# Performance work log

Hardware: AMD Instinct MI355X
Metric: run time of the kernel (lower is better)

The kernel has to match this reference:

```python
import jax, jax.numpy as jnp
import numpy as np

B, C, H, W = 16, 256, 56, 56
HID = C * 2            # modifier_expansion = 2
GROUPS = 8             # min(8, HID//4)
K = 3                  # inner_steps
LR = 0.01              # exp(log(inner_lr))
RATIO = 0.25           # spatial_mask_ratio
GN_EPS = 1e-5


def setup_inputs() -> dict:
    key = jax.random.key(0)
    ks = jax.random.split(key, 12)
    x = jax.random.normal(ks[0], (B, C, H, W), jnp.float32)
    # modifier params (1x1 convs stored as 2D matrices) + GroupNorm affine
    conv1_w = jax.random.normal(ks[1], (HID, C), jnp.float32) / np.sqrt(C)
    gn_gamma = 1.0 + 0.1 * jax.random.normal(ks[2], (HID,), jnp.float32)
    gn_beta = 0.1 * jax.random.normal(ks[3], (HID,), jnp.float32)
    conv2_w = jax.random.normal(ks[4], (C, HID), jnp.float32) / np.sqrt(HID)
    # surprise reconstructor (bottleneck = C//4)
    recon_w1 = jax.random.normal(ks[5], (C // 4, C), jnp.float32) / np.sqrt(C)
    recon_w2 = jax.random.normal(ks[6], (C, C // 4), jnp.float32) / np.sqrt(C // 4)
    # gate MLP
    gate_w1 = jax.random.normal(ks[7], (C // 4, C), jnp.float32) / np.sqrt(C)
    gate_b1 = jnp.zeros((C // 4,), jnp.float32)
    gate_w2 = jax.random.normal(ks[8], (1, C // 4), jnp.float32) / np.sqrt(C // 4)
    gate_b2 = jnp.zeros((1,), jnp.float32)
    residual_scale = jnp.asarray(0.05, jnp.float32)
    # EMA buffers (eval mode: frozen)
    running_mean = 0.05 * jax.random.normal(ks[9], (C,), jnp.float32)
    running_var = 1.0 + 0.05 * jax.random.uniform(ks[10], (C,), jnp.float32)
    # spatial masks: exactly int(H*W*RATIO) zeroed positions per sample, one mask
    # per inner update step (only steps 0..K-2 affect the output)
    num_mask = int(H * W * RATIO)
    rng = np.random.default_rng(0)
    r = rng.random((K - 1, B, H * W))
    idx = np.argsort(r, axis=-1)[..., :num_mask]
    m = np.ones((K - 1, B, H * W), dtype=bool)
    np.put_along_axis(m, idx, False, axis=-1)
    masks = jnp.asarray(m.reshape(K - 1, B, 1, H, W))
    return dict(x=x, conv1_w=conv1_w, gn_gamma=gn_gamma, gn_beta=gn_beta,
                conv2_w=conv2_w, recon_w1=recon_w1, recon_w2=recon_w2,
                gate_w1=gate_w1, gate_b1=gate_b1, gate_w2=gate_w2,
                gate_b2=gate_b2, residual_scale=residual_scale,
                running_mean=running_mean, running_var=running_var, masks=masks)


def _group_norm(h, gamma, beta):
    b = h.shape[0]
    hg = h.reshape(b, GROUPS, HID // GROUPS, H, W)
    mu = hg.mean(axis=(2, 3, 4), keepdims=True)
    var = hg.var(axis=(2, 3, 4), keepdims=True)  # biased, matching torch GN
    hg = (hg - mu) * jax.lax.rsqrt(var + GN_EPS)
    return hg.reshape(b, HID, H, W) * gamma[None, :, None, None] + beta[None, :, None, None]


def _modifier(feat, w1, gamma, beta, w2):
    # Conv2d 1x1 (no bias) -> GroupNorm -> GELU -> [Dropout2d: identity in eval] -> Conv2d 1x1
    h = jnp.einsum('bchw,oc->bohw', feat, w1)
    h = jax.nn.gelu(_group_norm(h, gamma, beta), approximate=False)
    return jnp.einsum('bohw,co->bchw', h, w2)


def _surprise(y, mask, rw1, rw2, rm, rv):
    mf = mask.astype(y.dtype)                       # [B,1,H,W]
    my = y * mf
    h = jax.nn.gelu(jnp.einsum('bchw,oc->bohw', my, rw1), approximate=False)
    rec = jnp.einsum('bohw,co->bchw', h, rw2)
    inv = 1.0 - mf
    recon = (((rec - y) ** 2) * inv).sum() / (inv.sum() * C + 1e-8)
    n = y.shape[0] * y.shape[2] * y.shape[3]
    cm = y.mean(axis=(0, 2, 3))                     # [C]
    cv = ((y - cm[None, :, None, None]) ** 2).sum(axis=(0, 2, 3)) / (n - 1)  # unbiased
    consist = ((cm - rm) ** 2).mean() + ((cv / (rv + 1e-8) - 1.0) ** 2).mean()
    return recon + 0.1 * consist


def reference(x, conv1_w, gn_gamma, gn_beta, conv2_w, recon_w1, recon_w2,
              gate_w1, gate_b1, gate_w2, gate_b2, residual_scale,
              running_mean, running_var, masks):
    feat = jax.lax.stop_gradient(x)  # feat_inner = features.detach()
    params = (conv1_w, gn_gamma, gn_beta, conv2_w)

    def inner_loss(p, mask):
        m = _modifier(feat, *p)
        return _surprise(m + feat, mask, recon_w1, recon_w2, running_mean, running_var)

    # TTT inner loop: K-1 SGD updates on the modifier params; updates are
    # stop_gradient'ed so the outer Jacobian wrt initial params is identity,
    # matching torch's .data in-place update with create_graph=False.
    for step in range(K - 1):
        g = jax.grad(inner_loss)(params, masks[step])
        params = tuple(p - LR * jax.lax.stop_gradient(gi) for p, gi in zip(params, g))

    modification = _modifier(x, *params)  # final forward uses non-detached features

    pooled = x.mean(axis=(2, 3))                                    # [B,C]
    gh = jax.nn.gelu(pooled @ gate_w1.T + gate_b1, approximate=False)
    gate = jax.nn.sigmoid(gh @ gate_w2.T + gate_b2)[:, :, None, None]  # [B,1,1,1]

    return x + residual_scale * gate * modification
```

## Files before the change

kernel.cpp:

```cpp
#include <hip/hip_runtime.h>
#include <math.h>


#define BB    16
#define CC    256
#define HWW   3136
#define NTOT  (BB*HWW)
#define HIDD  512
#define NGRP  8
#define GMSZ  (64*HWW)
#define C4    64
#define LRATE 0.01f
#define SKW   32
#define CHUNK (NTOT/SKW)
#define NV8   (HWW/8)
#define FSTR  132

#define EP_STORE    0
#define EP_ADDFEAT  1
#define EP_T1H      2
#define EP_DYREC    3
#define EP_DT1      4
#define EP_DYFIN    5
#define EP_H1STAT   6
#define EP_YADDSTAT 7
#define EP_GNB1     8
#define EP_OUT      9

typedef unsigned short u16;
typedef __attribute__((ext_vector_type(8))) short bf16x8;
typedef __attribute__((ext_vector_type(4))) float f32x4;

__device__ __forceinline__ float bf2f(u16 u){
  return __uint_as_float(((unsigned)u)<<16);
}
__device__ __forceinline__ u16 f2bf(float f){
  unsigned u = __float_as_uint(f);
  u += 0x7FFFu + ((u>>16)&1u);
  return (u16)(u>>16);
}
__device__ __forceinline__ float gelu_f(float x){
  return 0.5f*x*(1.0f+erff(x*0.70710678118654752f));
}
__device__ __forceinline__ float rcp_f(float x){ return __builtin_amdgcn_rcpf(x); }
__device__ __forceinline__ float gelu_fast(float x){
  float x2 = x*x;
  float u = 0.7978845608f*x*fmaf(0.044715f, x2, 1.0f);
  float t = 1.0f - 2.0f*rcp_f(__expf(2.0f*u)+1.0f);
  return 0.5f*x*(1.0f+t);
}
__device__ __forceinline__ float gelu_g_fast(float x){
  float x2 = x*x;
  float u = 0.7978845608f*x*fmaf(0.044715f, x2, 1.0f);
  float t = 1.0f - 2.0f*rcp_f(__expf(2.0f*u)+1.0f);
  float du = 0.7978845608f*fmaf(0.134145f, x2, 1.0f);
  return fmaf(0.5f*x*(1.0f-t*t), du, 0.5f*(1.0f+t));
}
__device__ __forceinline__ float blk_sum(float v, float* sm){
  #pragma unroll
  for (int o=32;o>0;o>>=1) v += __shfl_down(v,o);
  if ((threadIdx.x & 63)==0) sm[threadIdx.x>>6] = v;
  __syncthreads();
  float r = sm[0]+sm[1]+sm[2]+sm[3];
  __syncthreads();
  return r;
}
__device__ __forceinline__ uint4 pack8(const ushort* e){
  uint4 v;
  v.x = (unsigned)e[0] | ((unsigned)e[1]<<16);
  v.y = (unsigned)e[2] | ((unsigned)e[3]<<16);
  v.z = (unsigned)e[4] | ((unsigned)e[5]<<16);
  v.w = (unsigned)e[6] | ((unsigned)e[7]<<16);
  return v;
}
__device__ __forceinline__ void up8(uint4 v, float* f){
  f[0]=bf2f((u16)(v.x&0xFFFFu)); f[1]=bf2f((u16)(v.x>>16));
  f[2]=bf2f((u16)(v.y&0xFFFFu)); f[3]=bf2f((u16)(v.y>>16));
  f[4]=bf2f((u16)(v.z&0xFFFFu)); f[5]=bf2f((u16)(v.z>>16));
  f[6]=bf2f((u16)(v.w&0xFFFFu)); f[7]=bf2f((u16)(v.w>>16));
}
__device__ __forceinline__ uint4 pk8(const float* f){
  uint4 v;
  v.x=(unsigned)f2bf(f[0])|((unsigned)f2bf(f[1])<<16);
  v.y=(unsigned)f2bf(f[2])|((unsigned)f2bf(f[3])<<16);
  v.z=(unsigned)f2bf(f[4])|((unsigned)f2bf(f[5])<<16);
  v.w=(unsigned)f2bf(f[6])|((unsigned)f2bf(f[7])<<16);
  return v;
}

__global__ void k_detect_dtype(const u16* __restrict__ xs, int* flag){
  if (threadIdx.x || blockIdx.x) return;
  int plaus = 0;
  for (int i=0;i<256;i+=2){
    float f = bf2f(xs[i]);
    float a = fabsf(f);
    if (isfinite(f) && a < 32.0f && a > 1e-5f) plaus++;
  }
  *flag = (plaus >= 64) ? 1 : 0;
}
__global__ void k_detect_mask(const unsigned char* __restrict__ m, int* flag){
  if (threadIdx.x || blockIdx.x) return;
  unsigned char mx=0; int nz0=0,nz1=0,nz2=0,nz3=0;
  for (int i=0;i<256;i++){
    unsigned char v=m[i]; if (v>mx) mx=v;
    if (v){ int r=i&3; if(r==0)nz0=1; else if(r==1)nz1=1; else if(r==2)nz2=1; else nz3=1; }
  }
  int f;
  if (mx<=1) f = (nz1|nz2|nz3) ? 0 : 1;
  else       f = (!nz0 && !nz1) ? 3 : 2;
  *flag=f;
}
__global__ void k_report(u16* out, float v){
  if (threadIdx.x==0 && blockIdx.x==0) out[0] = f2bf(v);
}

__global__ void k_cvt(const void* __restrict__ src, float* __restrict__ dst, int n,
                      const int* __restrict__ dtf){
  int i = blockIdx.x*256 + threadIdx.x;
  if (i>=n) return;
  if (*dtf) dst[i] = bf2f(((const u16*)src)[i]);
  else      dst[i] = ((const float*)src)[i];
}
__global__ void k_wcvt(const float* __restrict__ src, u16* __restrict__ d,
                       u16* __restrict__ dT, int R, int Cc){
  int i = blockIdx.x*256+threadIdx.x;
  if (i >= R*Cc) return;
  int r = i/Cc, c = i - r*Cc;
  u16 v = f2bf(src[i]);
  d[i] = v;
  if (dT) dT[(size_t)c*R + r] = v;
}

__global__ void k_expand(const unsigned char* __restrict__ mraw, const int* __restrict__ flag,
                         float* __restrict__ mf, float* __restrict__ zc){
  __shared__ float sm[4];
  int i = blockIdx.x*256 + threadIdx.x;
  int f = *flag;
  float v;
  if (f==1)      v = (((const int*)mraw)[i] != 0) ? 1.f : 0.f;
  else if (f==0) v = (mraw[i] != 0) ? 1.f : 0.f;
  else if (f==2) v = (((const u16*)mraw)[i] != 0) ? 1.f : 0.f;
  else           v = (((const float*)mraw)[i] != 0.f) ? 1.f : 0.f;
  mf[i] = v;
  float S = blk_sum(1.f - v, sm);
  if (threadIdx.x==0) atomicAdd(&zc[blockIdx.x/196], S);
}

template<int MASKX,int EPI,int XDYN,int E0DYN,int XGN>
__global__ __launch_bounds__(256) void k_gemm_mfma(
    const u16* __restrict__ A, const void* __restrict__ Xv, u16* __restrict__ Out,
    int K, const int* __restrict__ xdt, const float* __restrict__ mf,
    const void* __restrict__ e0, const float* __restrict__ e1,
    const float* __restrict__ e2, u16* __restrict__ o2, float* __restrict__ o3,
    const float* __restrict__ xmu, const float* __restrict__ xpg)
{
  __shared__ __align__(16) u16 Ws[64*42];
  __shared__ __align__(16) u16 Xs[128*42];
  const int t = threadIdx.x;
  const int w = t >> 6, lane = t & 63;
  const int col = lane & 15, quad = lane >> 4;
  const int M = (int)gridDim.y << 6;
  const int m0 = blockIdx.y << 6, n0 = blockIdx.x << 7;
  const int isbx = XDYN ? *xdt : 1;
  const u16*   Xb = (const u16*)Xv;
  const float* Xf = (const float*)Xv;
  const int wrow = t >> 2, wkq = (t & 3) * 8;
  const int xn   = 2*(t & 63);
  const int xq   = t >> 6;
  const int gn0  = n0 + xn;
  const int xb_  = gn0 / HWW;
  const int xs_  = gn0 - xb_*HWW;

  f32x4 acc[4][2];
  #pragma unroll
  for (int i=0;i<4;i++){
    #pragma unroll
    for (int j=0;j<2;j++) acc[i][j] = (f32x4)(0.0f);
  }

  for (int k0=0; k0<K; k0+=32){
    {
      uint4 v = *(const uint4*)(A + (size_t)(m0+wrow)*K + k0 + wkq);
      *(uint4*)(Ws + wrow*42 + wkq) = v;
    }
    {
      ushort e[16];
      size_t base = ((size_t)xb_*K + k0 + xq*8)*HWW + xs_;
      if (isbx){
        #pragma unroll
        for (int j=0;j<8;j++){
          unsigned v = *(const unsigned*)(Xb + base + (size_t)j*HWW);
          if (XGN){
            const int o  = k0 + xq*8 + j;
            const int bg = xb_*NGRP + (o>>6);
            const float mu_ = xmu[bg], rs_ = xmu[128+bg];
            const float ga_ = xpg[o],  be_ = xpg[512+o];
            float f0 = bf2f((u16)(v & 0xFFFFu));
            float f1 = bf2f((u16)(v >> 16));
            f0 = fmaf((f0-mu_)*rs_, ga_, be_);
            f1 = fmaf((f1-mu_)*rs_, ga_, be_);
            f0 = (XGN==2) ? gelu_f(f0) : gelu_fast(f0);
            f1 = (XGN==2) ? gelu_f(f1) : gelu_fast(f1);
            e[j]   = f2bf(f0);
            e[8+j] = f2bf(f1);
          } else {
            e[j]   = (ushort)(v & 0xFFFFu);
            e[8+j] = (ushort)(v >> 16);
          }
        }
      } else {
        #pragma unroll
        for (int j=0;j<8;j++){
          float2 f = *(const float2*)(Xf + base + (size_t)j*HWW);
          e[j]   = f2bf(f.x);
          e[8+j] = f2bf(f.y);
        }
      }
      if (MASKX){
        if (mf[gn0]   == 0.f){
          #pragma unroll
          for (int j=0;j<8;j++) e[j] = 0;
        }
        if (mf[gn0+1] == 0.f){
          #pragma unroll
          for (int j=0;j<8;j++) e[8+j] = 0;
        }
      }
      *(uint4*)(Xs + xn*42     + xq*8) = pack8(e);
      *(uint4*)(Xs + (xn+1)*42 + xq*8) = pack8(e+8);
    }
    __syncthreads();
    bf16x8 af[4], bfr[2];
    #pragma unroll
    for (int mi=0;mi<4;mi++)
      af[mi] = *(const bf16x8*)(Ws + (mi*16+col)*42 + quad*8);
    #pragma unroll
    for (int nj=0;nj<2;nj++)
      bfr[nj] = *(const bf16x8*)(Xs + (w*32+nj*16+col)*42 + quad*8);
    #pragma unroll
    for (int mi=0;mi<4;mi++){
      #pragma unroll
      for (int nj=0;nj<2;nj++)
        acc[mi][nj] = __builtin_amdgcn_mfma_f32_16x16x32_bf16(af[mi], bfr[nj], acc[mi][nj], 0,0,0);
    }
    __syncthreads();
  }
  const int isb0 = E0DYN ? *xdt : 1;
  float* fst  = (float*)Xs;
  float* sred = (float*)Ws;
  const int row16 = t >> 4;
  const int cb    = (t & 15) * 8;
  const int nb8   = n0 + cb;
  const int b8    = nb8 / HWW;
  const int sb8   = nb8 - b8*HWW;
  const int bA    = n0 / HWW, bB = (n0+127)/HWW;
  const int g     = m0 >> 6;

  if (EPI==EP_H1STAT){ if (t<4) sred[t]=0.f; }
  if (EPI==EP_YADDSTAT){ for (int i=t;i<128;i+=256) sred[i]=0.f; }
  if (EPI==EP_GNB1){ for (int i=t;i<132;i+=256) sred[i]=0.f; }
  if (EPI==EP_H1STAT||EPI==EP_YADDSTAT||EPI==EP_GNB1) __syncthreads();

  float dscale=0.f, gmul=0.f, muT=0.f, rT=0.f;
  if (EPI==EP_DYREC) dscale = 2.0f / (e1[0]*(float)CC + 1e-8f);
  if (EPI==EP_OUT)   gmul = e2[0]*e1[b8];
  if (EPI==EP_GNB1){ muT = e1[b8*NGRP+g]; rT = e1[128+b8*NGRP+g]; }

  #pragma unroll
  for (int mi=0;mi<4;mi++){
    #pragma unroll
    for (int nj=0;nj<2;nj++){
      #pragma unroll
      for (int r=0;r<4;r++)
        fst[(quad*4+r)*FSTR + w*32 + nj*16 + col] = acc[mi][nj][r];
    }
    __syncthreads();
    const int m = m0 + mi*16 + row16;
    const size_t oidx = ((size_t)b8*M + m)*HWW + sb8;
    float v[8];
    {
      const float* frow = fst + row16*FSTR + cb;
      float4 p0 = *(const float4*)frow;
      float4 p1 = *(const float4*)(frow+4);
      v[0]=p0.x; v[1]=p0.y; v[2]=p0.z; v[3]=p0.w;
      v[4]=p1.x; v[5]=p1.y; v[6]=p1.z; v[7]=p1.w;
    }

    if (EPI==EP_STORE){
      *(uint4*)(Out+oidx) = pk8(v);
    }
    else if (EPI==EP_ADDFEAT){
      float xv[8];
      if (isb0) up8(*(const uint4*)((const u16*)e0+oidx), xv);
      else {
        float4 a0 = *(const float4*)((const float*)e0+oidx);
        float4 a1 = *(const float4*)((const float*)e0+oidx+4);
        xv[0]=a0.x; xv[1]=a0.y; xv[2]=a0.z; xv[3]=a0.w;
        xv[4]=a1.x; xv[5]=a1.y; xv[6]=a1.z; xv[7]=a1.w;
      }
      #pragma unroll
      for (int j=0;j<8;j++) v[j] += xv[j];
      *(uint4*)(Out+oidx) = pk8(v);
    }
    else if (EPI==EP_T1H){
      *(uint4*)(Out+oidx) = pk8(v);
      float gv[8];
      #pragma unroll
      for (int j=0;j<8;j++) gv[j] = gelu_fast(v[j]);
      *(uint4*)(o2+oidx) = pk8(gv);
    }
    else if (EPI==EP_DYREC){
      float yv[8], mfv[8];
      up8(*(const uint4*)((const u16*)e0+oidx), yv);
      float4 f0 = *(const float4*)(mf+nb8);
      float4 f1 = *(const float4*)(mf+nb8+4);
      mfv[0]=f0.x; mfv[1]=f0.y; mfv[2]=f0.z; mfv[3]=f0.w;
      mfv[4]=f1.x; mfv[5]=f1.y; mfv[6]=f1.z; mfv[7]=f1.w;
      #pragma unroll
      for (int j=0;j<8;j++) v[j] = (v[j]-yv[j])*(1.0f-mfv[j])*dscale;
      *(uint4*)(Out+oidx) = pk8(v);
    }
    else if (EPI==EP_DT1){
      float tv[8];
      up8(*(const uint4*)((const u16*)e0+oidx), tv);
      #pragma unroll
      for (int j=0;j<8;j++) v[j] = v[j]*gelu_g_fast(tv[j]);
      *(uint4*)(Out+oidx) = pk8(v);
    }
    else if (EPI==EP_DYFIN){
      float yv[8], dv[8], mfv[8];
      up8(*(const uint4*)((const u16*)e0+oidx), yv);
      up8(*(const uint4*)(Out+oidx), dv);
      float4 f0 = *(const float4*)(mf+nb8);
      float4 f1 = *(const float4*)(mf+nb8+4);
      mfv[0]=f0.x; mfv[1]=f0.y; mfv[2]=f0.z; mfv[3]=f0.w;
      mfv[4]=f1.x; mfv[5]=f1.y; mfv[6]=f1.z; mfv[7]=f1.w;
      const float c1 = e1[m], c2 = e2[m];
      #pragma unroll
      for (int j=0;j<8;j++) v[j] = mfv[j]*v[j] - dv[j] + c1 + c2*yv[j];
      *(uint4*)(Out+oidx) = pk8(v);
    }
    else if (EPI==EP_H1STAT){
      *(uint4*)(Out+oidx) = pk8(v);
      float s=0.f, q=0.f;
      #pragma unroll
      for (int j=0;j<8;j++){ s += v[j]; q = fmaf(v[j],v[j],q); }
      float s0 = (b8==bA)?s:0.f, q0 = (b8==bA)?q:0.f;
      float s1v = s-s0, q1v = q-q0;
      #pragma unroll
      for (int o=1;o<64;o<<=1){
        s0 += __shfl_xor(s0,o); q0 += __shfl_xor(q0,o);
        s1v += __shfl_xor(s1v,o); q1v += __shfl_xor(q1v,o);
      }
      if (lane==0){
        atomicAdd(&sred[0], s0); atomicAdd(&sred[1], q0);
        atomicAdd(&sred[2], s1v); atomicAdd(&sred[3], q1v);
      }
    }
    else if (EPI==EP_YADDSTAT){
      float xv[8];
      if (isb0) up8(*(const uint4*)((const u16*)e0+oidx), xv);
      else {
        float4 a0 = *(const float4*)((const float*)e0+oidx);
        float4 a1 = *(const float4*)((const float*)e0+oidx+4);
        xv[0]=a0.x; xv[1]=a0.y; xv[2]=a0.z; xv[3]=a0.w;
        xv[4]=a1.x; xv[5]=a1.y; xv[6]=a1.z; xv[7]=a1.w;
      }
      float s=0.f, q=0.f;
      #pragma unroll
      for (int j=0;j<8;j++){
        v[j] += xv[j];
        s += v[j]; q = fmaf(v[j],v[j],q);
      }
      *(uint4*)(Out+oidx) = pk8(v);
      #pragma unroll
      for (int o=1;o<16;o<<=1){ s += __shfl_xor(s,o); q += __shfl_xor(q,o); }
      if ((t&15)==0){
        atomicAdd(&sred[mi*16+row16],    s);
        atomicAdd(&sred[64+mi*16+row16], q);
      }
    }
    else if (EPI==EP_GNB1){
      float hv[8];
      up8(*(const uint4*)((const u16*)e0+oidx), hv);
      const float go = e2[m], beo = e2[HIDD+m];
      float dB=0.f, dG=0.f, sS=0.f, sQ=0.f;
      #pragma unroll
      for (int j=0;j<8;j++){
        float hn   = (hv[j]-muT)*rT;
        float ghat = fmaf(hn, go, beo);
        float dgh  = v[j]*gelu_g_fast(ghat);
        float dhn  = dgh*go;
        v[j] = dhn;
        dB += dgh; dG = fmaf(dgh,hn,dG);
        sS += dhn; sQ = fmaf(dhn,hn,sQ);
      }
      *(uint4*)(Out+oidx) = pk8(v);
      #pragma unroll
      for (int o=1;o<16;o<<=1){ dB += __shfl_xor(dB,o); dG += __shfl_xor(dG,o); }
      if ((t&15)==0){
        atomicAdd(&sred[mi*16+row16],    dB);
        atomicAdd(&sred[64+mi*16+row16], dG);
      }
      float s0 = (b8==bA)?sS:0.f, q0 = (b8==bA)?sQ:0.f;
      float s1v = sS-s0, q1v = sQ-q0;
      #pragma unroll
      for (int o=1;o<64;o<<=1){
        s0 += __shfl_xor(s0,o); q0 += __shfl_xor(q0,o);
        s1v += __shfl_xor(s1v,o); q1v += __shfl_xor(q1v,o);
      }
      if (lane==0){
        atomicAdd(&sred[128], s0); atomicAdd(&sred[129], q0);
        atomicAdd(&sred[130], s1v); atomicAdd(&sred[131], q1v);
      }
    }
    else if (EPI==EP_OUT){
      float xv[8];
      if (isb0){
        up8(*(const uint4*)((const u16*)e0+oidx), xv);
        #pragma unroll
        for (int j=0;j<8;j++) v[j] = xv[j] + gmul*v[j];
        *(uint4*)(Out+oidx) = pk8(v);
      } else {
        float4 a0 = *(const float4*)((const float*)e0+oidx);
        float4 a1 = *(const float4*)((const float*)e0+oidx+4);
        float4 r0, r1;
        r0.x = a0.x + gmul*v[0]; r0.y = a0.y + gmul*v[1];
        r0.z = a0.z + gmul*v[2]; r0.w = a0.w + gmul*v[3];
        r1.x = a1.x + gmul*v[4]; r1.y = a1.y + gmul*v[5];
        r1.z = a1.z + gmul*v[6]; r1.w = a1.w + gmul*v[7];
        *(float4*)((float*)Out+oidx)   = r0;
        *(float4*)((float*)Out+oidx+4) = r1;
      }
    }
    __syncthreads();
  }

  if (EPI==EP_H1STAT){
    if (t==0){
      atomicAdd(&o3[bA*NGRP+g],     sred[0]);
      atomicAdd(&o3[128+bA*NGRP+g], sred[1]);
    }
    if (t==1 && bB!=bA){
      atomicAdd(&o3[bB*NGRP+g],     sred[2]);
      atomicAdd(&o3[128+bB*NGRP+g], sred[3]);
    }
  }
  if (EPI==EP_YADDSTAT){
    if (t<64){
      atomicAdd(&o3[m0+t],    sred[t]);
      atomicAdd(&o3[CC+m0+t], sred[64+t]);
    }
  }
  if (EPI==EP_GNB1){
    if (t<64){
      atomicAdd(&o3[m0+t],     sred[64+t]);
      atomicAdd(&o3[512+m0+t], sred[t]);
    }
    if (t==64){
      atomicAdd(&o3[1024+bA*NGRP+g], sred[128]);
      atomicAdd(&o3[1152+bA*NGRP+g], sred[129]);
    }
    if (t==65 && bB!=bA){
      atomicAdd(&o3[1024+bB*NGRP+g], sred[130]);
      atomicAdd(&o3[1152+bB*NGRP+g], sred[131]);
    }
  }
}

template<int QDYN, int GNB2>
__global__ __launch_bounds__(256) void k_wgrad_mfma(
    const u16* __restrict__ P, const void* __restrict__ Qv, float* __restrict__ part,
    int CHP, int CHQ, const int* __restrict__ xdt, int ntx,
    const u16* __restrict__ h1, const float* __restrict__ musig,
    const float* __restrict__ red)
{
  __shared__ __align__(16) u16 Ps[64*42];
  __shared__ __align__(16) u16 Qs[64*42];
  const int f = blockIdx.x;
  const int j = f >> 3;
  const int sk = (f & 7) + ((j >> 5) << 3);
  const int tile = j & 31;
  const int ty = tile / ntx;
  const int m0 = (tile - ty*ntx) << 6;
  const int n0 = ty << 6;
  const int t = threadIdx.x;
  const int w = t >> 6, lane = t & 63;
  const int col = lane & 15, quad = lane >> 4;
  const int isbq = QDYN ? *xdt : 1;
  const u16*   Qb = (const u16*)Qv;
  const float* Qf = (const float*)Qv;
  const int srow = (t & 127) >> 1;
  const int ssq  = ((t & 127) & 1) * 16;
  f32x4 acc[2][2];
  #pragma unroll
  for (int i=0;i<2;i++){
    #pragma unroll
    for (int jj=0;jj<2;jj++) acc[i][jj] = (f32x4)(0.0f);
  }
  const int mbase = (w & 1)*32, nbase = (w >> 1)*32;

  for (int kb = sk*CHUNK; kb < sk*CHUNK + CHUNK; kb += 32){
    const int b = kb / HWW;
    const int s = kb - b*HWW;
    if (t < 128){
      size_t off = ((size_t)b*CHP + m0+srow)*HWW + s + ssq;
      uint4 v0 = *(const uint4*)(P + off);
      uint4 v1 = *(const uint4*)(P + off + 8);
      if (GNB2){
        const int bg = b*NGRP + (m0>>6);
        const float mu_ = musig[bg], r_ = musig[128+bg];
        const float a1 = red[1024+bg]*(1.0f/GMSZ);
        const float a2 = red[1152+bg]*(1.0f/GMSZ);
        uint4 h0 = *(const uint4*)(h1 + off);
        uint4 h1v = *(const uint4*)(h1 + off + 8);
        float fd[8], fh[8];
        up8(v0, fd); up8(h0, fh);
        #pragma unroll
        for (int q2=0;q2<8;q2++){ float hn=(fh[q2]-mu_)*r_; fd[q2]=r_*(fd[q2]-a1-hn*a2); }
        v0 = pk8(fd);
        up8(v1, fd); up8(h1v, fh);
        #pragma unroll
        for (int q2=0;q2<8;q2++){ float hn=(fh[q2]-mu_)*r_; fd[q2]=r_*(fd[q2]-a1-hn*a2); }
        v1 = pk8(fd);
      }
      *(uint4*)(Ps + srow*42 + ssq)     = v0;
      *(uint4*)(Ps + srow*42 + ssq + 8) = v1;
    } else {
      size_t off = ((size_t)b*CHQ + n0+srow)*HWW + s + ssq;
      if (isbq){
        uint4 v0 = *(const uint4*)(Qb + off);
        uint4 v1 = *(const uint4*)(Qb + off + 8);
        *(uint4*)(Qs + srow*42 + ssq)     = v0;
        *(uint4*)(Qs + srow*42 + ssq + 8) = v1;
      } else {
        ushort e[16];
        #pragma unroll
        for (int g2=0; g2<4; g2++){
          float4 ff = *(const float4*)(Qf + off + g2*4);
          e[g2*4+0]=f2bf(ff.x); e[g2*4+1]=f2bf(ff.y); e[g2*4+2]=f2bf(ff.z); e[g2*4+3]=f2bf(ff.w);
        }
        *(uint4*)(Qs + srow*42 + ssq)     = pack8(e);
        *(uint4*)(Qs + srow*42 + ssq + 8) = pack8(e+8);
      }
    }
    __syncthreads();
    bf16x8 pa[2], qb[2];
    #pragma unroll
    for (int a=0;a<2;a++)
      pa[a] = *(const bf16x8*)(Ps + (mbase + a*16 + col)*42 + quad*8);
    #pragma unroll
    for (int bb=0;bb<2;bb++)
      qb[bb] = *(const bf16x8*)(Qs + (nbase + bb*16 + col)*42 + quad*8);
    #pragma unroll
    for (int a=0;a<2;a++){
      #pragma unroll
      for (int bb=0;bb<2;bb++)
        acc[a][bb] = __builtin_amdgcn_mfma_f32_16x16x32_bf16(pa[a], qb[bb], acc[a][bb], 0,0,0);
    }
    __syncthreads();
  }
  float* dst = part + (size_t)sk*CHP*CHQ;
  #pragma unroll
  for (int a=0;a<2;a++){
    #pragma unroll
    for (int bb=0;bb<2;bb++){
      #pragma unroll
      for (int r=0;r<4;r++){
        const int m = m0 + mbase + a*16 + quad*4 + r;
        const int n = n0 + nbase + bb*16 + col;
        dst[(size_t)m*CHQ + n] = acc[a][bb][r];
      }
    }
  }
}
__global__ void k_wgrad_reduce(const float* __restrict__ part, float* __restrict__ dW, int n){
  int i = blockIdx.x*256+threadIdx.x;
  if (i>=n) return;
  float s=0;
  #pragma unroll
  for (int k=0;k<SKW;k++) s += part[(size_t)k*n + i];
  dW[i]=s;
}

__global__ void k_gn_finalize(const float* gsum, const float* gsumsq, float* mu, float* rsig){
  int i = threadIdx.x; if (i>=BB*NGRP) return;
  float m = gsum[i]*(1.0f/GMSZ);
  float v = gsumsq[i]*(1.0f/GMSZ) - m*m;
  v = fmaxf(v, 0.0f);
  mu[i]=m; rsig[i]=rsqrtf(v+1e-5f);
}
template<int FAST>
__global__ void k_gelu_fwd(const u16* __restrict__ src, u16* __restrict__ dst,
    const float* __restrict__ mu, const float* __restrict__ rsig,
    const float* __restrict__ pg, const float* __restrict__ pb){
  int bo = blockIdx.x;
  int b = bo>>9, o = bo&511, bg = b*NGRP + (o>>6);
  float m = mu[bg], r = rsig[bg], g = pg[o], be = pb[o];
  const uint4* ps = (const uint4*)(src + (size_t)bo*HWW);
  uint4* pd = (uint4*)(dst + (size_t)bo*HWW);
  for (int i=threadIdx.x;i<NV8;i+=256){
    float f[8]; up8(ps[i], f);
    #pragma unroll
    for (int j=0;j<8;j++){
      float gh = fmaf((f[j]-m)*r, g, be);
      f[j] = FAST ? gelu_fast(gh) : gelu_f(gh);
    }
    pd[i] = pk8(f);
  }
}

__global__ void k_y_finalize(const float* cmsum, const float* cmsq,
    const float* rmf, const float* rvf, float* coefA, float* coefB){
  int c = threadIdx.x; if (c>=CC) return;
  float cm = cmsum[c]*(1.0f/NTOT);
  float cv = (cmsq[c] - (float)NTOT*cm*cm)*(1.0f/(NTOT-1));
  float rvp = rvf[c] + 1e-8f;
  float gcm = 0.2f*(cm - rmf[c])*(1.0f/CC);
  float gcv = 0.2f*(cv/rvp - 1.0f)/(rvp*(float)CC);
  coefA[c] = gcm*(1.0f/NTOT) - 2.0f*gcv*cm*(1.0f/(NTOT-1));
  coefB[c] = 2.0f*gcv*(1.0f/(NTOT-1));
}

__global__ void k_gn_bwd1(u16* __restrict__ dA, const u16* __restrict__ h1,
    const float* mu, const float* rsig, const float* pg, const float* pb,
    float* dGa, float* dBe, float* s1, float* s2){
  __shared__ float sm[4];
  int bo = blockIdx.x;
  int b = bo>>9, o = bo&511, bg = b*NGRP + (o>>6);
  float m = mu[bg], r = rsig[bg], g = pg[o], be = pb[o];
  uint4* pa = (uint4*)(dA + (size_t)bo*HWW);
  const uint4* ph = (const uint4*)(h1 + (size_t)bo*HWW);
  float sb=0, sg=0, t1=0, t2=0;
  for (int i=threadIdx.x;i<NV8;i+=256){
    float fa[8], fh[8]; up8(pa[i], fa); up8(ph[i], fh);
    #pragma unroll
    for (int j=0;j<8;j++){
      float hn = (fh[j]-m)*r;
      float ghat = fmaf(hn,g,be);
      float dgh = fa[j]*gelu_g_fast(ghat);
      float dhn = dgh*g;
      fa[j] = dhn;
      sb += dgh; sg = fmaf(dgh,hn,sg); t1 += dhn; t2 = fmaf(dhn,hn,t2);
    }
    pa[i] = pk8(fa);
  }
  float S;
  S = blk_sum(sb,sm); if (threadIdx.x==0) atomicAdd(&dBe[o], S);
  S = blk_sum(sg,sm); if (threadIdx.x==0) atomicAdd(&dGa[o], S);
  S = blk_sum(t1,sm); if (threadIdx.x==0) atomicAdd(&s1[bg], S);
  S = blk_sum(t2,sm); if (threadIdx.x==0) atomicAdd(&s2[bg], S);
}
__global__ void k_gn_bwd2(u16* __restrict__ dA, const u16* __restrict__ h1,
    const float* mu, const float* rsig, const float* s1, const float* s2){
  int bo = blockIdx.x;
  int b = bo>>9, o = bo&511, bg = b*NGRP + (o>>6);
  float m = mu[bg], r = rsig[bg];
  float a1 = s1[bg]*(1.0f/GMSZ), a2 = s2[bg]*(1.0f/GMSZ);
  uint4* pa = (uint4*)(dA + (size_t)bo*HWW);
  const uint4* ph = (const uint4*)(h1 + (size_t)bo*HWW);
  for (int i=threadIdx.x;i<NV8;i+=256){
    float fa[8], fh[8]; up8(pa[i], fa); up8(ph[i], fh);
    #pragma unroll
    for (int j=0;j<8;j++){
      float hn = (fh[j]-m)*r;
      fa[j] = r*(fa[j] - a1 - hn*a2);
    }
    pa[i] = pk8(fa);
  }
}

__global__ void k_update(float* pw1, float* pw2, float* pg, float* pb,
    const float* dW1, const float* dW2, const float* dGa, const float* dBe){
  int i = blockIdx.x*256+threadIdx.x;
  if (i < HIDD*CC){ pw1[i] -= LRATE*dW1[i]; pw2[i] -= LRATE*dW2[i]; }
  if (i < HIDD){ pg[i] -= LRATE*dGa[i]; pb[i] -= LRATE*dBe[i]; }
}

__global__ void k_pool(const void* __restrict__ xv, const int* __restrict__ dtf, float* pooled){
  __shared__ float sm[4];
  int bc = blockIdx.x;
  int isb = *dtf;
  float s=0;
  if (isb){
    const uint4* p = (const uint4*)((const u16*)xv + (size_t)bc*HWW);
    for (int i=threadIdx.x;i<NV8;i+=256){
      float f[8]; up8(p[i], f);
      #pragma unroll
      for (int j=0;j<8;j++) s+=f[j];
    }
  } else {
    const float4* p = (const float4*)((const float*)xv + (size_t)bc*HWW);
    for (int i=threadIdx.x;i<HWW/4;i+=256){
      float4 f = p[i];
      s += f.x+f.y+f.z+f.w;
    }
  }
  float S = blk_sum(s,sm);
  if (threadIdx.x==0) pooled[bc]=S*(1.0f/HWW);
}
__global__ void k_gate(const float* __restrict__ pooled, const float* __restrict__ gw1,
    const float* __restrict__ gb1, const float* __restrict__ gw2, const float* __restrict__ gb2,
    float* gate){
  int b = blockIdx.x, j = threadIdx.x;
  float acc = gb1[j];
  const float* pr = pooled + b*CC;
  for (int c=0;c<CC;c++) acc = fmaf(pr[c], gw1[j*CC+c], acc);
  float v = gelu_f(acc)*gw2[j];
  #pragma unroll
  for (int o=32;o>0;o>>=1) v += __shfl_down(v,o);
  if (j==0) gate[b] = 1.0f/(1.0f+expf(-(v+gb2[0])));
}

extern "C" void kernel_launch(void* const* d_in, const int* in_sizes, int n_in,
                              void* d_out, int out_size, void* d_ws, size_t ws_size,
                              hipStream_t stream)
{
  const void* x_in   = d_in[0];
  const void* w1_in  = d_in[1];
  const void* g_in   = d_in[2];
  const void* b_in   = d_in[3];
  const void* w2_in  = d_in[4];
  const void* rw1_in = d_in[5];
  const void* rw2_in = d_in[6];
  const void* gw1_in = d_in[7];
  const void* gb1_in = d_in[8];
  const void* gw2_in = d_in[9];
  const void* gb2_in = d_in[10];
  const void* rs_in  = d_in[11];
  const void* rm_in  = d_in[12];
  const void* rv_in  = d_in[13];
  const void* mk_in  = d_in[14];
  (void)in_sizes; (void)n_in; (void)out_size;

  char* base = (char*)d_ws;
  size_t off = 0;
  auto alloc = [&](size_t bytes)->char*{
    char* p = base+off; off = (off+bytes+255)&~(size_t)255; return p;
  };
  u16* ybuf = (u16*)alloc((size_t)CC*NTOT*2);
  u16* dY   = (u16*)alloc((size_t)CC*NTOT*2);
  u16* Ab   = (u16*)alloc((size_t)HIDD*NTOT*2);
  u16* t1b  = (u16*)alloc((size_t)C4*NTOT*2);
  u16* hb   = (u16*)alloc((size_t)C4*NTOT*2);
  u16* h1rc = ybuf;
  float* part = (float*)ybuf;
  float* mfb  = (float*)alloc((size_t)2*NTOT*4);
  float* pw1  = (float*)alloc(131072*4);
  float* pw2  = (float*)alloc(131072*4);
  float* dW1  = (float*)alloc(131072*4);
  float* dW2  = (float*)alloc(131072*4);
  u16* wb1   = (u16*)alloc(131072*2);
  u16* wb2   = (u16*)alloc(131072*2);
  u16* wb2T  = (u16*)alloc(131072*2);
  u16* rwb1  = (u16*)alloc(16384*2);
  u16* rwb1T = (u16*)alloc(16384*2);
  u16* rwb2  = (u16*)alloc(16384*2);
  u16* rwb2T = (u16*)alloc(16384*2);
  float* pg   = (float*)alloc(512*4);
  float* pb   = (float*)alloc(512*4);
  float* rw1f = (float*)alloc(16384*4);
  float* rw2f = (float*)alloc(16384*4);
  float* gw1f = (float*)alloc(16384*4);
  float* gb1f = (float*)alloc(64*4);
  float* gw2f = (float*)alloc(64*4);
  float* gb2f = (float*)alloc(256);
  float* rmf  = (float*)alloc(256*4);
  float* rvf  = (float*)alloc(256*4);
  float* rsf  = (float*)alloc(256);
  float* gsum   = (float*)alloc(512);
  float* gsumsq = (float*)alloc(512);
  float* mu     = (float*)alloc(512);
  float* rsig   = (float*)alloc(512);
  float* cmsum  = (float*)alloc(1024);
  float* cmsq   = (float*)alloc(1024);
  float* coefA  = (float*)alloc(1024);
  float* coefB  = (float*)alloc(1024);
  float* dGa    = (float*)alloc(2048);
  float* dBe    = (float*)alloc(2048);
  float* s1     = (float*)alloc(512);
  float* s2     = (float*)alloc(512);
  float* pooled = (float*)alloc(16384);
  float* gate   = (float*)alloc(256);
  float* zc     = (float*)alloc(256);
  int*   dtf    = (int*)alloc(256);
  int*   mkf    = (int*)alloc(256);

  if (off > ws_size){
    k_report<<<1,64,0,stream>>>((u16*)d_out, (float)(ws_size>>20));
    return;
  }
  u16* h1p = nullptr;
  if (off + (size_t)HIDD*NTOT*2 <= ws_size)
    h1p = (u16*)alloc((size_t)HIDD*NTOT*2);

  k_detect_dtype<<<1,1,0,stream>>>((const u16*)x_in, dtf);
  k_detect_mask<<<1,1,0,stream>>>((const unsigned char*)mk_in, mkf);
  #define CVT(src,dst,n) k_cvt<<<((n)+255)/256,256,0,stream>>>(src,dst,(n),dtf)
  CVT(w1_in,  pw1,  131072);
  CVT(g_in,   pg,   512);
  CVT(b_in,   pb,   512);
  CVT(w2_in,  pw2,  131072);
  CVT(rw1_in, rw1f, 16384);
  CVT(rw2_in, rw2f, 16384);
  CVT(gw1_in, gw1f, 16384);
  CVT(gb1_in, gb1f, 64);
  CVT(gw2_in, gw2f, 64);
  CVT(gb2_in, gb2f, 1);
  CVT(rs_in,  rsf,  1);
  CVT(rm_in,  rmf,  256);
  CVT(rv_in,  rvf,  256);
  #undef CVT
  k_wcvt<<<512,256,0,stream>>>(pw1, wb1, 0,     HIDD, CC);
  k_wcvt<<<512,256,0,stream>>>(pw2, wb2, wb2T,  CC, HIDD);
  k_wcvt<<<64,256,0,stream>>>(rw1f, rwb1, rwb1T, C4, CC);
  k_wcvt<<<64,256,0,stream>>>(rw2f, rwb2, rwb2T, CC, C4);
  hipMemsetAsync(zc, 0, 8, stream);
  k_expand<<<392,256,0,stream>>>((const unsigned char*)mk_in, mkf, mfb, zc);

  for (int s=0; s<2; s++){
    const float* mfs = mfb + s*NTOT;
    u16* h1dst = h1p ? h1p : Ab;
    hipMemsetAsync(gsum, 0, 1024, stream);
    k_gemm_mfma<0,EP_H1STAT,1,0,0><<<dim3(392,8),256,0,stream>>>(wb1, x_in, h1dst, CC, dtf, 0,0,0,0,0, gsum, 0,0);
    k_gn_finalize<<<1,128,0,stream>>>(gsum, gsumsq, mu, rsig);
    k_gelu_fwd<1><<<BB*HIDD,256,0,stream>>>(h1dst, Ab, mu, rsig, pg, pb);
    hipMemsetAsync(cmsum, 0, 2048, stream);
    k_gemm_mfma<0,EP_YADDSTAT,0,1,0><<<dim3(392,4),256,0,stream>>>(wb2, Ab, ybuf, HIDD, dtf, 0, x_in, 0,0,0, cmsum, 0,0);
    k_y_finalize<<<1,256,0,stream>>>(cmsum, cmsq, rmf, rvf, coefA, coefB);
    k_gemm_mfma<1,EP_T1H,0,0,0><<<dim3(392,1),256,0,stream>>>(rwb1, ybuf, t1b, CC, dtf, mfs, 0,0,0, hb, 0, 0,0);
    k_gemm_mfma<0,EP_DYREC,0,0,0><<<dim3(392,4),256,0,stream>>>(rwb2, hb, dY, C4, dtf, mfs, ybuf, zc+s, 0,0, 0, 0,0);
    k_gemm_mfma<0,EP_DT1,0,0,0><<<dim3(392,1),256,0,stream>>>(rwb2T, dY, hb, CC, dtf, 0, t1b, 0,0,0, 0, 0,0);
    k_gemm_mfma<0,EP_DYFIN,0,0,0><<<dim3(392,4),256,0,stream>>>(rwb1T, hb, dY, C4, dtf, mfs, ybuf, coefA, coefB, 0, 0, 0,0);
    k_wgrad_mfma<0,0><<<dim3(32*SKW),256,0,stream>>>(dY, Ab, part, CC, HIDD, dtf, 4, 0,0,0);
    k_wgrad_reduce<<<512,256,0,stream>>>(part, dW2, 131072);
    hipMemsetAsync(dGa, 0, 5120, stream);
    if (h1p){
      k_gemm_mfma<0,EP_GNB1,0,0,0><<<dim3(392,8),256,0,stream>>>(wb2T, dY, Ab, CC, dtf, 0, h1p, mu, pg, 0, dGa, 0,0);
      k_wgrad_mfma<1,1><<<dim3(32*SKW),256,0,stream>>>(Ab, x_in, part, HIDD, CC, dtf, 8, h1p, mu, dGa);
    } else {
      k_gemm_mfma<0,EP_STORE,0,0,0><<<dim3(392,8),256,0,stream>>>(wb2T, dY, Ab, CC, dtf, 0,0,0,0,0, 0, 0,0);
      k_gemm_mfma<0,EP_H1STAT,1,0,0><<<dim3(392,8),256,0,stream>>>(wb1, x_in, h1rc, CC, dtf, 0,0,0,0,0, gsum, 0,0);
      k_gn_bwd1<<<BB*HIDD,256,0,stream>>>(Ab, h1rc, mu, rsig, pg, pb, dGa, dBe, s1, s2);
      k_gn_bwd2<<<BB*HIDD,256,0,stream>>>(Ab, h1rc, mu, rsig, s1, s2);
      k_wgrad_mfma<1,0><<<dim3(32*SKW),256,0,stream>>>(Ab, x_in, part, HIDD, CC, dtf, 8, 0,0,0);
    }
    k_wgrad_reduce<<<512,256,0,stream>>>(part, dW1, 131072);
    k_update<<<512,256,0,stream>>>(pw1, pw2, pg, pb, dW1, dW2, dGa, dBe);
    k_wcvt<<<512,256,0,stream>>>(pw1, wb1, 0,    HIDD, CC);
    k_wcvt<<<512,256,0,stream>>>(pw2, wb2, wb2T, CC, HIDD);
  }

  k_pool<<<BB*CC,256,0,stream>>>(x_in, dtf, pooled);
  k_gate<<<BB,64,0,stream>>>(pooled, gw1f, gb1f, gw2f, gb2f, gate);

  hipMemsetAsync(gsum, 0, 1024, stream);
  k_gemm_mfma<0,EP_H1STAT,1,0,0><<<dim3(392,8),256,0,stream>>>(wb1, x_in, Ab, CC, dtf, 0,0,0,0,0, gsum, 0,0);
  k_gn_finalize<<<1,128,0,stream>>>(gsum, gsumsq, mu, rsig);
  k_gemm_mfma<0,EP_OUT,0,1,2><<<dim3(392,4),256,0,stream>>>(wb2, Ab, (u16*)d_out, HIDD, dtf, 0, x_in, gate, rsf, 0, 0, mu, pg);
}
```

Baseline: 1.192 ms.

## Fuse GroupNorm+GELU into GEMM and wgrad operand loads, drop gelu_fwd pass

When the h1 buffer is available, the separate GroupNorm+GELU forward kernel is removed. The normalize+GELU is instead applied on the fly while loading h1 tiles into shared memory in both the y-GEMM and the dW2 weight-gradient kernel, which saves a full read/write pass over the hidden activation. The final output GEMM also switches from exact GELU to the fast approximation, and the LDS row stride changes from 42 to 40 elements. In exchange, GELU is recomputed in two kernels, and the approximate GELU plus the new stride may change accuracy and LDS bank-conflict behaviour.

```diff
diff --git a/kernel.cpp b/kernel.cpp
--- a/kernel.cpp
+++ b/kernel.cpp
@@ -154,8 +154,8 @@
     const float* __restrict__ e2, u16* __restrict__ o2, float* __restrict__ o3,
     const float* __restrict__ xmu, const float* __restrict__ xpg)
 {
-  __shared__ __align__(16) u16 Ws[64*42];
-  __shared__ __align__(16) u16 Xs[128*42];
+  __shared__ __align__(16) u16 Ws[64*40];
+  __shared__ __align__(16) u16 Xs[128*40];
   const int t = threadIdx.x;
   const int w = t >> 6, lane = t & 63;
   const int col = lane & 15, quad = lane >> 4;
@@ -181,7 +181,7 @@
   for (int k0=0; k0<K; k0+=32){
     {
       uint4 v = *(const uint4*)(A + (size_t)(m0+wrow)*K + k0 + wkq);
-      *(uint4*)(Ws + wrow*42 + wkq) = v;
+      *(uint4*)(Ws + wrow*40 + wkq) = v;
     }
     {
       ushort e[16];
@@ -197,10 +197,8 @@
             const float ga_ = xpg[o],  be_ = xpg[512+o];
             float f0 = bf2f((u16)(v & 0xFFFFu));
             float f1 = bf2f((u16)(v >> 16));
-            f0 = fmaf((f0-mu_)*rs_, ga_, be_);
-            f1 = fmaf((f1-mu_)*rs_, ga_, be_);
-            f0 = (XGN==2) ? gelu_f(f0) : gelu_fast(f0);
-            f1 = (XGN==2) ? gelu_f(f1) : gelu_fast(f1);
+            f0 = gelu_fast(fmaf((f0-mu_)*rs_, ga_, be_));
+            f1 = gelu_fast(fmaf((f1-mu_)*rs_, ga_, be_));
             e[j]   = f2bf(f0);
             e[8+j] = f2bf(f1);
           } else {
@@ -226,17 +224,17 @@
           for (int j=0;j<8;j++) e[8+j] = 0;
         }
       }
-      *(uint4*)(Xs + xn*42     + xq*8) = pack8(e);
-      *(uint4*)(Xs + (xn+1)*42 + xq*8) = pack8(e+8);
+      *(uint4*)(Xs + xn*40     + xq*8) = pack8(e);
+      *(uint4*)(Xs + (xn+1)*40 + xq*8) = pack8(e+8);
     }
     __syncthreads();
     bf16x8 af[4], bfr[2];
     #pragma unroll
     for (int mi=0;mi<4;mi++)
-      af[mi] = *(const bf16x8*)(Ws + (mi*16+col)*42 + quad*8);
+      af[mi] = *(const bf16x8*)(Ws + (mi*16+col)*40 + quad*8);
     #pragma unroll
     for (int nj=0;nj<2;nj++)
-      bfr[nj] = *(const bf16x8*)(Xs + (w*32+nj*16+col)*42 + quad*8);
+      bfr[nj] = *(const bf16x8*)(Xs + (w*32+nj*16+col)*40 + quad*8);
     #pragma unroll
     for (int mi=0;mi<4;mi++){
       #pragma unroll
@@ -468,15 +466,15 @@
   }
 }
 
-template<int QDYN, int GNB2>
+template<int QDYN, int GNB2, int QGN>
 __global__ __launch_bounds__(256) void k_wgrad_mfma(
     const u16* __restrict__ P, const void* __restrict__ Qv, float* __restrict__ part,
     int CHP, int CHQ, const int* __restrict__ xdt, int ntx,
     const u16* __restrict__ h1, const float* __restrict__ musig,
-    const float* __restrict__ red)
+    const float* __restrict__ red, const float* __restrict__ qpg)
 {
-  __shared__ __align__(16) u16 Ps[64*42];
-  __shared__ __align__(16) u16 Qs[64*42];
+  __shared__ __align__(16) u16 Ps[64*40];
+  __shared__ __align__(16) u16 Qs[64*40];
   const int f = blockIdx.x;
   const int j = f >> 3;
   const int sk = (f & 7) + ((j >> 5) << 3);
@@ -524,15 +522,30 @@
         for (int q2=0;q2<8;q2++){ float hn=(fh[q2]-mu_)*r_; fd[q2]=r_*(fd[q2]-a1-hn*a2); }
         v1 = pk8(fd);
       }
-      *(uint4*)(Ps + srow*42 + ssq)     = v0;
-      *(uint4*)(Ps + srow*42 + ssq + 8) = v1;
+      *(uint4*)(Ps + srow*40 + ssq)     = v0;
+      *(uint4*)(Ps + srow*40 + ssq + 8) = v1;
     } else {
       size_t off = ((size_t)b*CHQ + n0+srow)*HWW + s + ssq;
       if (isbq){
         uint4 v0 = *(const uint4*)(Qb + off);
         uint4 v1 = *(const uint4*)(Qb + off + 8);
-        *(uint4*)(Qs + srow*42 + ssq)     = v0;
-        *(uint4*)(Qs + srow*42 + ssq + 8) = v1;
+        if (QGN){
+          const int o  = n0 + srow;
+          const int bg = b*NGRP + (o>>6);
+          const float mu_ = musig[bg], rs_ = musig[128+bg];
+          const float ga_ = qpg[o], be_ = qpg[512+o];
+          float fq[8];
+          up8(v0, fq);
+          #pragma unroll
+          for (int q2=0;q2<8;q2++) fq[q2] = gelu_fast(fmaf((fq[q2]-mu_)*rs_, ga_, be_));
+          v0 = pk8(fq);
+          up8(v1, fq);
+          #pragma unroll
+          for (int q2=0;q2<8;q2++) fq[q2] = gelu_fast(fmaf((fq[q2]-mu_)*rs_, ga_, be_));
+          v1 = pk8(fq);
+        }
+        *(uint4*)(Qs + srow*40 + ssq)     = v0;
+        *(uint4*)(Qs + srow*40 + ssq + 8) = v1;
       } else {
         ushort e[16];
         #pragma unroll
@@ -540,18 +553,18 @@
           float4 ff = *(const float4*)(Qf + off + g2*4);
           e[g2*4+0]=f2bf(ff.x); e[g2*4+1]=f2bf(ff.y); e[g2*4+2]=f2bf(ff.z); e[g2*4+3]=f2bf(ff.w);
         }
-        *(uint4*)(Qs + srow*42 + ssq)     = pack8(e);
-        *(uint4*)(Qs + srow*42 + ssq + 8) = pack8(e+8);
+        *(uint4*)(Qs + srow*40 + ssq)     = pack8(e);
+        *(uint4*)(Qs + srow*40 + ssq + 8) = pack8(e+8);
       }
     }
     __syncthreads();
     bf16x8 pa[2], qb[2];
     #pragma unroll
     for (int a=0;a<2;a++)
-      pa[a] = *(const bf16x8*)(Ps + (mbase + a*16 + col)*42 + quad*8);
+      pa[a] = *(const bf16x8*)(Ps + (mbase + a*16 + col)*40 + quad*8);
     #pragma unroll
     for (int bb=0;bb<2;bb++)
-      qb[bb] = *(const bf16x8*)(Qs + (nbase + bb*16 + col)*42 + quad*8);
+      qb[bb] = *(const bf16x8*)(Qs + (nbase + bb*16 + col)*40 + quad*8);
     #pragma unroll
     for (int a=0;a<2;a++){
       #pragma unroll
@@ -824,26 +837,34 @@
     hipMemsetAsync(gsum, 0, 1024, stream);
     k_gemm_mfma<0,EP_H1STAT,1,0,0><<<dim3(392,8),256,0,stream>>>(wb1, x_in, h1dst, CC, dtf, 0,0,0,0,0, gsum, 0,0);
     k_gn_finalize<<<1,128,0,stream>>>(gsum, gsumsq, mu, rsig);
-    k_gelu_fwd<1><<<BB*HIDD,256,0,stream>>>(h1dst, Ab, mu, rsig, pg, pb);
     hipMemsetAsync(cmsum, 0, 2048, stream);
-    k_gemm_mfma<0,EP_YADDSTAT,0,1,0><<<dim3(392,4),256,0,stream>>>(wb2, Ab, ybuf, HIDD, dtf, 0, x_in, 0,0,0, cmsum, 0,0);
+    if (h1p){
+      k_gemm_mfma<0,EP_YADDSTAT,0,1,1><<<dim3(392,4),256,0,stream>>>(wb2, h1p, ybuf, HIDD, dtf, 0, x_in, 0,0,0, cmsum, mu, pg);
+    } else {
+      k_gelu_fwd<1><<<BB*HIDD,256,0,stream>>>(Ab, Ab, mu, rsig, pg, pb);
+      k_gemm_mfma<0,EP_YADDSTAT,0,1,0><<<dim3(392,4),256,0,stream>>>(wb2, Ab, ybuf, HIDD, dtf, 0, x_in, 0,0,0, cmsum, 0,0);
+    }
     k_y_finalize<<<1,256,0,stream>>>(cmsum, cmsq, rmf, rvf, coefA, coefB);
     k_gemm_mfma<1,EP_T1H,0,0,0><<<dim3(392,1),256,0,stream>>>(rwb1, ybuf, t1b, CC, dtf, mfs, 0,0,0, hb, 0, 0,0);
     k_gemm_mfma<0,EP_DYREC,0,0,0><<<dim3(392,4),256,0,stream>>>(rwb2, hb, dY, C4, dtf, mfs, ybuf, zc+s, 0,0, 0, 0,0);
     k_gemm_mfma<0,EP_DT1,0,0,0><<<dim3(392,1),256,0,stream>>>(rwb2T, dY, hb, CC, dtf, 0, t1b, 0,0,0, 0, 0,0);
     k_gemm_mfma<0,EP_DYFIN,0,0,0><<<dim3(392,4),256,0,stream>>>(rwb1T, hb, dY, C4, dtf, mfs, ybuf, coefA, coefB, 0, 0, 0,0);
-    k_wgrad_mfma<0,0><<<dim3(32*SKW),256,0,stream>>>(dY, Ab, part, CC, HIDD, dtf, 4, 0,0,0);
+    if (h1p){
+      k_wgrad_mfma<0,0,1><<<dim3(32*SKW),256,0,stream>>>(dY, h1p, part, CC, HIDD, dtf, 4, 0, mu, 0, pg);
+    } else {
+      k_wgrad_mfma<0,0,0><<<dim3(32*SKW),256,0,stream>>>(dY, Ab, part, CC, HIDD, dtf, 4, 0,0,0,0);
+    }
     k_wgrad_reduce<<<512,256,0,stream>>>(part, dW2, 131072);
     hipMemsetAsync(dGa, 0, 5120, stream);
     if (h1p){
       k_gemm_mfma<0,EP_GNB1,0,0,0><<<dim3(392,8),256,0,stream>>>(wb2T, dY, Ab, CC, dtf, 0, h1p, mu, pg, 0, dGa, 0,0);
-      k_wgrad_mfma<1,1><<<dim3(32*SKW),256,0,stream>>>(Ab, x_in, part, HIDD, CC, dtf, 8, h1p, mu, dGa);
+      k_wgrad_mfma<1,1,0><<<dim3(32*SKW),256,0,stream>>>(Ab, x_in, part, HIDD, CC, dtf, 8, h1p, mu, dGa, 0);
     } else {
       k_gemm_mfma<0,EP_STORE,0,0,0><<<dim3(392,8),256,0,stream>>>(wb2T, dY, Ab, CC, dtf, 0,0,0,0,0, 0, 0,0);
       k_gemm_mfma<0,EP_H1STAT,1,0,0><<<dim3(392,8),256,0,stream>>>(wb1, x_in, h1rc, CC, dtf, 0,0,0,0,0, gsum, 0,0);
       k_gn_bwd1<<<BB*HIDD,256,0,stream>>>(Ab, h1rc, mu, rsig, pg, pb, dGa, dBe, s1, s2);
       k_gn_bwd2<<<BB*HIDD,256,0,stream>>>(Ab, h1rc, mu, rsig, s1, s2);
-      k_wgrad_mfma<1,0><<<dim3(32*SKW),256,0,stream>>>(Ab, x_in, part, HIDD, CC, dtf, 8, 0,0,0);
+      k_wgrad_mfma<1,0,0><<<dim3(32*SKW),256,0,stream>>>(Ab, x_in, part, HIDD, CC, dtf, 8, 0,0,0,0);
     }
     k_wgrad_reduce<<<512,256,0,stream>>>(part, dW1, 131072);
     k_update<<<512,256,0,stream>>>(pw1, pw2, pg, pb, dW1, dW2, dGa, dBe);
@@ -857,5 +878,5 @@
   hipMemsetAsync(gsum, 0, 1024, stream);
   k_gemm_mfma<0,EP_H1STAT,1,0,0><<<dim3(392,8),256,0,stream>>>(wb1, x_in, Ab, CC, dtf, 0,0,0,0,0, gsum, 0,0);
   k_gn_finalize<<<1,128,0,stream>>>(gsum, gsumsq, mu, rsig);
-  k_gemm_mfma<0,EP_OUT,0,1,2><<<dim3(392,4),256,0,stream>>>(wb2, Ab, (u16*)d_out, HIDD, dtf, 0, x_in, gate, rsf, 0, 0, mu, pg);
-}
+  k_gemm_mfma<0,EP_OUT,0,1,1><<<dim3(392,4),256,0,stream>>>(wb2, Ab, (u16*)d_out, HIDD, dtf, 0, x_in, gate, rsf, 0, 0, mu, pg);
+}
```

New measurement: 1.247 ms. 4.6% more time.
